# Performance work log

Measured on AMD Instinct MI355X. Metric: run time of the kernel, lower is better.

## Reference

```python
import jax, jax.numpy as jnp
import numpy as np

N_NODES = 50000
N_EDGES = 600000
N_PATHS = 3
IN_DIM = 128
OUT_DIM = 128  # out_size(16) * heads(8)
SEM_HID = 128


def setup_inputs() -> dict:
    key = jax.random.key(0)
    ks = jax.random.split(key, 8)
    h = jax.random.normal(ks[0], (N_NODES, IN_DIM), jnp.float32)
    edge_src = jax.random.randint(ks[1], (N_PATHS, N_EDGES), 0, N_NODES, dtype=jnp.int32)
    edge_dst = jax.random.randint(ks[2], (N_PATHS, N_EDGES), 0, N_NODES, dtype=jnp.int32)
    W_gc = jax.random.normal(ks[3], (N_PATHS, IN_DIM, OUT_DIM), jnp.float32) * (1.0 / np.sqrt(IN_DIM))
    b_gc = jnp.zeros((N_PATHS, OUT_DIM), jnp.float32)
    w1 = jax.random.normal(ks[4], (OUT_DIM, SEM_HID), jnp.float32) * (1.0 / np.sqrt(OUT_DIM))
    b1 = jnp.zeros((SEM_HID,), jnp.float32)
    w2 = jax.random.normal(ks[5], (SEM_HID, 1), jnp.float32) * (1.0 / np.sqrt(SEM_HID))
    return {"h": h, "W_gc": W_gc, "b_gc": b_gc, "w1": w1, "b1": b1, "w2": w2,
            "edge_src": edge_src, "edge_dst": edge_dst}


def reference(h, W_gc, b_gc, w1, b1, w2, edge_src, edge_dst):
    n = h.shape[0]

    def graph_conv(W, b, src, dst):
        # DGL GraphConv, norm='both': D_out^{-1/2} message -> sum -> D_in^{-1/2}, + bias
        ones = jnp.ones(src.shape, h.dtype)
        deg_out = jax.ops.segment_sum(ones, src, num_segments=n)
        deg_in = jax.ops.segment_sum(ones, dst, num_segments=n)
        x = h * jax.lax.rsqrt(jnp.maximum(deg_out, 1.0))[:, None]
        x = x @ W  # [N, OUT_DIM]
        agg = jax.ops.segment_sum(x[src], dst, num_segments=n)
        return agg * jax.lax.rsqrt(jnp.maximum(deg_in, 1.0))[:, None] + b

    # z: [N, P, D] stacked per-metapath embeddings
    z = jax.vmap(graph_conv, in_axes=(0, 0, 0, 0), out_axes=1)(W_gc, b_gc, edge_src, edge_dst)
    # semantic attention: mean over nodes of per-(node,path) scores
    w = jnp.mean(jnp.tanh(z @ w1 + b1) @ w2, axis=0)  # [P, 1]
    beta = jax.nn.softmax(w, axis=0)                   # [P, 1]
    return jnp.sum(beta * z, axis=1)                   # [N, D]
```

## Files before the change

kernel.cpp:

```cpp
#include <hip/hip_runtime.h>
#include <math.h>

#define N_NODES 50000
#define N_EDGES 600000
#define N_PATHS 3
#define DIM 128
#define NROWS_ALL (N_PATHS * N_NODES)
#define NE_ALL (N_PATHS * N_EDGES)
#define SCAN_BLOCKS ((NROWS_ALL + 1023) / 1024)
#define NTILES_ALL (NROWS_ALL / 16)
#define NTILES_N (N_NODES / 16)

#define HB_BINS 16384
#define HB_RANGES 4
#define HB_CHUNKS 24
#define CHUNK_E (N_EDGES / HB_CHUNKS)

typedef __attribute__((ext_vector_type(8))) short bf16x8;
typedef __attribute__((ext_vector_type(4))) float f32x4;

__device__ __forceinline__ unsigned short f2bf(float f) {
    unsigned u = __float_as_uint(f);
    u += 0x7FFF + ((u >> 16) & 1);
    return (unsigned short)(u >> 16);
}
__device__ __forceinline__ float tanh_fast(float x) {
    return 1.0f - 2.0f / (__expf(2.0f * x) + 1.0f);
}

__global__ void conv_h(const float* __restrict__ h, unsigned int* __restrict__ hb) {
    int i = blockIdx.x * blockDim.x + threadIdx.x;
    if (i >= N_NODES * DIM / 8) return;
    const float4* h4 = (const float4*)h;
    float4 a = h4[2 * i], b = h4[2 * i + 1];
    uint4 o;
    o.x = f2bf(a.x) | ((unsigned)f2bf(a.y) << 16);
    o.y = f2bf(a.z) | ((unsigned)f2bf(a.w) << 16);
    o.z = f2bf(b.x) | ((unsigned)f2bf(b.y) << 16);
    o.w = f2bf(b.z) | ((unsigned)f2bf(b.w) << 16);
    ((uint4*)hb)[i] = o;
}

__global__ void conv_w(const float* __restrict__ W_gc, const float* __restrict__ w1,
                       uint4* __restrict__ wsw) {
    int i = blockIdx.x * blockDim.x + threadIdx.x;
    if (i >= (N_PATHS + 1) * 2048) return;
    int mat = i >> 11;
    int rem = i & 2047;
    int frag = rem >> 6, lane = rem & 63;
    int n0 = frag >> 2, q = frag & 3;
    int quad = lane >> 4, m = lane & 15;
    int n = n0 * 16 + m;
    int kbase = q * 32 + quad * 8;
    const float* src = (mat < N_PATHS) ? (W_gc + (size_t)mat * DIM * DIM) : w1;
    unsigned short t[8];
#pragma unroll
    for (int j = 0; j < 8; ++j) t[j] = f2bf(src[(size_t)(kbase + j) * DIM + n]);
    uint4 o;
    o.x = t[0] | ((unsigned)t[1] << 16);
    o.y = t[2] | ((unsigned)t[3] << 16);
    o.z = t[4] | ((unsigned)t[5] << 16);
    o.w = t[6] | ((unsigned)t[7] << 16);
    wsw[i] = o;
}

__global__ __launch_bounds__(256) void hist_kernel(const int* __restrict__ esrc,
                                                   const int* __restrict__ edst,
                                                   int* __restrict__ pcnt_out,
                                                   int* __restrict__ pcnt_in) {
    __shared__ int bins[HB_BINS];
    int tid = threadIdx.x;
    {   int4* b4 = (int4*)bins;
        for (int i = tid; i < HB_BINS / 4; i += 256) b4[i] = make_int4(0, 0, 0, 0);
    }
    int b = blockIdx.x;
    int c = b % HB_CHUNKS;
    int r = (b / HB_CHUNKS) % HB_RANGES;
    int p = (b / (HB_CHUNKS * HB_RANGES)) % N_PATHS;
    int type = b / (HB_CHUNKS * HB_RANGES * N_PATHS);
    const int* ptr = (type == 0 ? esrc : edst) + (size_t)p * N_EDGES + c * CHUNK_E;
    int r0 = r * HB_BINS;
    __syncthreads();
    const int4* p4 = (const int4*)ptr;
    for (int i = tid * 2; i < CHUNK_E / 4; i += 512) {
        int4 a = p4[i];
        int4 bb = p4[i + 1];
        int l0 = a.x - r0;  if ((unsigned)l0 < HB_BINS) atomicAdd(&bins[l0], 1);
        int l1 = a.y - r0;  if ((unsigned)l1 < HB_BINS) atomicAdd(&bins[l1], 1);
        int l2 = a.z - r0;  if ((unsigned)l2 < HB_BINS) atomicAdd(&bins[l2], 1);
        int l3 = a.w - r0;  if ((unsigned)l3 < HB_BINS) atomicAdd(&bins[l3], 1);
        int l4 = bb.x - r0; if ((unsigned)l4 < HB_BINS) atomicAdd(&bins[l4], 1);
        int l5 = bb.y - r0; if ((unsigned)l5 < HB_BINS) atomicAdd(&bins[l5], 1);
        int l6 = bb.z - r0; if ((unsigned)l6 < HB_BINS) atomicAdd(&bins[l6], 1);
        int l7 = bb.w - r0; if ((unsigned)l7 < HB_BINS) atomicAdd(&bins[l7], 1);
    }
    __syncthreads();
    int bound = min(HB_BINS, N_NODES - r0);
    int* dst = (type == 0 ? pcnt_out : pcnt_in) + (size_t)c * NROWS_ALL + p * N_NODES + r0;
    const int4* b4 = (const int4*)bins;
    int4* d4 = (int4*)dst;
    for (int i = tid; i < bound / 4; i += 256) d4[i] = b4[i];
}

__global__ __launch_bounds__(256) void scan_pass1(const int* __restrict__ pcnt_out,
                                                  const int* __restrict__ pcnt_in,
                                                  int* __restrict__ cnt_out,
                                                  int* __restrict__ cnt_in,
                                                  float* __restrict__ sc_out,
                                                  int* __restrict__ partial) {
    __shared__ int lds[256];
    int t = threadIdx.x;
    int base = blockIdx.x * 1024 + t * 4;
    int4 ci = make_int4(0, 0, 0, 0);
    if (base < NROWS_ALL) {
        int4 co = make_int4(0, 0, 0, 0);
#pragma unroll
        for (int c = 0; c < HB_CHUNKS; ++c) {
            int4 vi = *(const int4*)(pcnt_in + (size_t)c * NROWS_ALL + base);
            int4 vo = *(const int4*)(pcnt_out + (size_t)c * NROWS_ALL + base);
            ci.x += vi.x; ci.y += vi.y; ci.z += vi.z; ci.w += vi.w;
            co.x += vo.x; co.y += vo.y; co.z += vo.z; co.w += vo.w;
        }
        *(int4*)(cnt_in + base) = ci;
        *(int4*)(cnt_out + base) = co;
        float4 sc;
        sc.x = rsqrtf(fmaxf((float)co.x, 1.0f));
        sc.y = rsqrtf(fmaxf((float)co.y, 1.0f));
        sc.z = rsqrtf(fmaxf((float)co.z, 1.0f));
        sc.w = rsqrtf(fmaxf((float)co.w, 1.0f));
        *(float4*)(sc_out + base) = sc;
    }
    int s = ci.x + ci.y + ci.z + ci.w;
    lds[t] = s; __syncthreads();
    for (int off = 1; off < 256; off <<= 1) {
        int u = (t >= off) ? lds[t - off] : 0;
        __syncthreads();
        lds[t] += u;
        __syncthreads();
    }
    if (t == 255) partial[blockIdx.x] = lds[255];
}

__global__ __launch_bounds__(256) void scan_pass2(int* __restrict__ partial) {
    __shared__ int lds[256];
    int t = threadIdx.x;
    int s = (t < SCAN_BLOCKS) ? partial[t] : 0;
    lds[t] = s; __syncthreads();
    for (int off = 1; off < 256; off <<= 1) {
        int u = (t >= off) ? lds[t - off] : 0;
        __syncthreads();
        lds[t] += u;
        __syncthreads();
    }
    if (t < SCAN_BLOCKS) partial[t] = lds[t] - s;
}

__global__ __launch_bounds__(256) void scan_pass3(const int* __restrict__ cnt,
                                                  const int* __restrict__ partial,
                                                  int* __restrict__ cursor,
                                                  int* __restrict__ pcnt_in) {
    __shared__ int lds[256];
    int t = threadIdx.x;
    int base = blockIdx.x * 1024 + t * 4;
    int4 v = make_int4(0, 0, 0, 0);
    if (base < NROWS_ALL) v = *(const int4*)(cnt + base);
    int s = v.x + v.y + v.z + v.w;
    lds[t] = s; __syncthreads();
    for (int off = 1; off < 256; off <<= 1) {
        int u = (t >= off) ? lds[t - off] : 0;
        __syncthreads();
        lds[t] += u;
        __syncthreads();
    }
    if (base < NROWS_ALL) {
        int run = partial[blockIdx.x] + lds[t] - s;
        int vv[4] = {v.x, v.y, v.z, v.w};
        int rb[4];
#pragma unroll
        for (int j = 0; j < 4; ++j) { cursor[base + j] = run; rb[j] = run; run += vv[j]; }
#pragma unroll
        for (int c = 0; c < HB_CHUNKS; ++c) {
            int4 pc = *(const int4*)(pcnt_in + (size_t)c * NROWS_ALL + base);
            *(int4*)(pcnt_in + (size_t)c * NROWS_ALL + base) = make_int4(rb[0], rb[1], rb[2], rb[3]);
            rb[0] += pc.x; rb[1] += pc.y; rb[2] += pc.z; rb[3] += pc.w;
        }
    }
}

__global__ __launch_bounds__(256) void fill2_kernel(const int* __restrict__ esrc,
                                                    const int* __restrict__ edst,
                                                    const int* __restrict__ pcnt_in,
                                                    unsigned short* __restrict__ col) {
    __shared__ int curs[HB_BINS];
    int tid = threadIdx.x;
    int b = blockIdx.x;
    int c = b % HB_CHUNKS;
    int r = (b / HB_CHUNKS) % HB_RANGES;
    int p = b / (HB_CHUNKS * HB_RANGES);
    int r0 = r * HB_BINS;
    int bound = min(HB_BINS, N_NODES - r0);
    const int* basep = pcnt_in + (size_t)c * NROWS_ALL + p * N_NODES + r0;
    for (int i = tid; i < bound; i += 256) curs[i] = basep[i];
    __syncthreads();
    const int4* sp4 = (const int4*)(esrc + (size_t)p * N_EDGES + c * CHUNK_E);
    const int4* dp4 = (const int4*)(edst + (size_t)p * N_EDGES + c * CHUNK_E);
    for (int i = tid * 2; i < CHUNK_E / 4; i += 512) {
        int4 dv0 = dp4[i];
        int4 dv1 = dp4[i + 1];
        int4 sv0 = sp4[i];
        int4 sv1 = sp4[i + 1];
        int l0 = dv0.x - r0; if ((unsigned)l0 < HB_BINS) { int pos = atomicAdd(&curs[l0], 1); col[pos] = (unsigned short)sv0.x; }
        int l1 = dv0.y - r0; if ((unsigned)l1 < HB_BINS) { int pos = atomicAdd(&curs[l1], 1); col[pos] = (unsigned short)sv0.y; }
        int l2 = dv0.z - r0; if ((unsigned)l2 < HB_BINS) { int pos = atomicAdd(&curs[l2], 1); col[pos] = (unsigned short)sv0.z; }
        int l3 = dv0.w - r0; if ((unsigned)l3 < HB_BINS) { int pos = atomicAdd(&curs[l3], 1); col[pos] = (unsigned short)sv0.w; }
        int l4 = dv1.x - r0; if ((unsigned)l4 < HB_BINS) { int pos = atomicAdd(&curs[l4], 1); col[pos] = (unsigned short)sv1.x; }
        int l5 = dv1.y - r0; if ((unsigned)l5 < HB_BINS) { int pos = atomicAdd(&curs[l5], 1); col[pos] = (unsigned short)sv1.y; }
        int l6 = dv1.z - r0; if ((unsigned)l6 < HB_BINS) { int pos = atomicAdd(&curs[l6], 1); col[pos] = (unsigned short)sv1.z; }
        int l7 = dv1.w - r0; if ((unsigned)l7 < HB_BINS) { int pos = atomicAdd(&curs[l7], 1); col[pos] = (unsigned short)sv1.w; }
    }
}

__global__ __launch_bounds__(256) void gather_kernel(const int* __restrict__ cursor,
                                                     const int* __restrict__ cnt_in,
                                                     const unsigned short* __restrict__ col,
                                                     const float* __restrict__ sc_out,
                                                     const uint4* __restrict__ hb4,
                                                     uint4* __restrict__ aggb4) {
    int wid = blockIdx.x * 4 + (threadIdx.x >> 6);
    int lane = threadIdx.x & 63;
    int ss = lane >> 4;
    int ln = lane & 15;
    if (wid >= NROWS_ALL) return;
    int p = wid / N_NODES;
    int beg = cursor[wid];
    int end = beg + cnt_in[wid];
    const float* scp = sc_out + p * N_NODES;
    float acc[8] = {};
    int e = beg + ss;
    for (; e + 4 < end; e += 8) {
        int s0 = col[e];
        int s1 = col[e + 4];
        float c0 = scp[s0];
        float c1 = scp[s1];
        uint4 v0 = hb4[s0 * 16 + ln];
        uint4 v1 = hb4[s1 * 16 + ln];
        acc[0] = fmaf(__uint_as_float(v0.x << 16),        c0, acc[0]);
        acc[1] = fmaf(__uint_as_float(v0.x & 0xFFFF0000u), c0, acc[1]);
        acc[2] = fmaf(__uint_as_float(v0.y << 16),        c0, acc[2]);
        acc[3] = fmaf(__uint_as_float(v0.y & 0xFFFF0000u), c0, acc[3]);
        acc[4] = fmaf(__uint_as_float(v0.z << 16),        c0, acc[4]);
        acc[5] = fmaf(__uint_as_float(v0.z & 0xFFFF0000u), c0, acc[5]);
        acc[6] = fmaf(__uint_as_float(v0.w << 16),        c0, acc[6]);
        acc[7] = fmaf(__uint_as_float(v0.w & 0xFFFF0000u), c0, acc[7]);
        acc[0] = fmaf(__uint_as_float(v1.x << 16),        c1, acc[0]);
        acc[1] = fmaf(__uint_as_float(v1.x & 0xFFFF0000u), c1, acc[1]);
        acc[2] = fmaf(__uint_as_float(v1.y << 16),        c1, acc[2]);
        acc[3] = fmaf(__uint_as_float(v1.y & 0xFFFF0000u), c1, acc[3]);
        acc[4] = fmaf(__uint_as_float(v1.z << 16),        c1, acc[4]);
        acc[5] = fmaf(__uint_as_float(v1.z & 0xFFFF0000u), c1, acc[5]);
        acc[6] = fmaf(__uint_as_float(v1.w << 16),        c1, acc[6]);
        acc[7] = fmaf(__uint_as_float(v1.w & 0xFFFF0000u), c1, acc[7]);
    }
    if (e < end) {
        int s0 = col[e];
        float c0 = scp[s0];
        uint4 v0 = hb4[s0 * 16 + ln];
        acc[0] = fmaf(__uint_as_float(v0.x << 16),        c0, acc[0]);
        acc[1] = fmaf(__uint_as_float(v0.x & 0xFFFF0000u), c0, acc[1]);
        acc[2] = fmaf(__uint_as_float(v0.y << 16),        c0, acc[2]);
        acc[3] = fmaf(__uint_as_float(v0.y & 0xFFFF0000u), c0, acc[3]);
        acc[4] = fmaf(__uint_as_float(v0.z << 16),        c0, acc[4]);
        acc[5] = fmaf(__uint_as_float(v0.z & 0xFFFF0000u), c0, acc[5]);
        acc[6] = fmaf(__uint_as_float(v0.w << 16),        c0, acc[6]);
        acc[7] = fmaf(__uint_as_float(v0.w & 0xFFFF0000u), c0, acc[7]);
    }
#pragma unroll
    for (int j = 0; j < 8; ++j) {
        acc[j] += __shfl_xor(acc[j], 16, 64);
        acc[j] += __shfl_xor(acc[j], 32, 64);
    }
    if (ss == 0) {
        uint4 o;
        o.x = f2bf(acc[0]) | ((unsigned)f2bf(acc[1]) << 16);
        o.y = f2bf(acc[2]) | ((unsigned)f2bf(acc[3]) << 16);
        o.z = f2bf(acc[4]) | ((unsigned)f2bf(acc[5]) << 16);
        o.w = f2bf(acc[6]) | ((unsigned)f2bf(acc[7]) << 16);
        int t = wid >> 4, m = wid & 15, q = ln >> 2, qd = ln & 3;
        aggb4[(size_t)t * 256 + q * 64 + qd * 16 + m] = o;
    }
}

__global__ __launch_bounds__(256, 4) void score_pass(const uint4* __restrict__ aggb4,
                                                     const uint4* __restrict__ wsw,
                                                     const int* __restrict__ cnt_in,
                                                     const float* __restrict__ b_gc,
                                                     const float* __restrict__ b1,
                                                     const float* __restrict__ w2,
                                                     float* __restrict__ scorep) {
    __shared__ float zS[4][16][132];
    int wave = threadIdx.x >> 6, lane = threadIdx.x & 63;
    int m = lane & 15, quad = lane >> 4;
    int t = blockIdx.x * 4 + wave;
    if (t >= NTILES_ALL) return;
    int r0 = t * 16;
    int p = r0 / N_NODES;
    const uint4* At = aggb4 + (size_t)t * 256 + lane;
    bf16x8 a[4];
#pragma unroll
    for (int q = 0; q < 4; ++q) a[q] = *(const bf16x8*)&At[q * 64];
    float s[4];
#pragma unroll
    for (int rg = 0; rg < 4; ++rg)
        s[rg] = rsqrtf(fmaxf((float)cnt_in[r0 + quad * 4 + rg], 1.0f));
    const uint4* Bp = wsw + (size_t)p * 2048 + lane;
    const float* bgc = b_gc + p * DIM;
    float (*zw)[132] = zS[wave];
#pragma unroll
    for (int n0 = 0; n0 < 8; ++n0) {
        f32x4 acc = {0.f, 0.f, 0.f, 0.f};
#pragma unroll
        for (int q = 0; q < 4; ++q) {
            bf16x8 b = *(const bf16x8*)&Bp[(n0 * 4 + q) * 64];
            acc = __builtin_amdgcn_mfma_f32_16x16x32_bf16(a[q], b, acc, 0, 0, 0);
        }
        int colj = n0 * 16 + m;
        float bias = bgc[colj];
#pragma unroll
        for (int rg = 0; rg < 4; ++rg)
            zw[quad * 4 + rg][colj] = acc[rg] * s[rg] + bias;
    }
    bf16x8 sa[4];
#pragma unroll
    for (int q = 0; q < 4; ++q) {
        const float* pr = &zw[m][q * 32 + quad * 8];
        float4 f0 = *(const float4*)pr;
        float4 f1 = *(const float4*)(pr + 4);
        bf16x8 tt;
        tt[0] = f2bf(f0.x); tt[1] = f2bf(f0.y); tt[2] = f2bf(f0.z); tt[3] = f2bf(f0.w);
        tt[4] = f2bf(f1.x); tt[5] = f2bf(f1.y); tt[6] = f2bf(f1.z); tt[7] = f2bf(f1.w);
        sa[q] = tt;
    }
    const uint4* W1 = wsw + (size_t)N_PATHS * 2048 + lane;
    float rsum[4] = {0.f, 0.f, 0.f, 0.f};
#pragma unroll
    for (int n0 = 0; n0 < 8; ++n0) {
        f32x4 acc = {0.f, 0.f, 0.f, 0.f};
#pragma unroll
        for (int q = 0; q < 4; ++q) {
            bf16x8 b = *(const bf16x8*)&W1[(n0 * 4 + q) * 64];
            acc = __builtin_amdgcn_mfma_f32_16x16x32_bf16(sa[q], b, acc, 0, 0, 0);
        }
        int colj = n0 * 16 + m;
        float bj = b1[colj], wj = w2[colj];
#pragma unroll
        for (int rg = 0; rg < 4; ++rg)
            rsum[rg] += tanh_fast(acc[rg] + bj) * wj;
    }
#pragma unroll
    for (int off = 1; off < 64; off <<= 1)
#pragma unroll
        for (int rg = 0; rg < 4; ++rg) rsum[rg] += __shfl_xor(rsum[rg], off, 64);
    if (lane == 0)
        scorep[t] = rsum[0] + rsum[1] + rsum[2] + rsum[3];
}

__global__ __launch_bounds__(1024) void beta_kernel(const float* __restrict__ scorep,
                                                    float* __restrict__ beta) {
    __shared__ float red[3][1024];
    int t = threadIdx.x;
    float a0 = 0.f, a1 = 0.f, a2 = 0.f;
    for (int i = t; i < NTILES_ALL; i += 1024) {
        float v = scorep[i];
        int p = (i * 16) / N_NODES;
        if (p == 0) a0 += v; else if (p == 1) a1 += v; else a2 += v;
    }
    red[0][t] = a0; red[1][t] = a1; red[2][t] = a2;
    __syncthreads();
    for (int off = 512; off > 0; off >>= 1) {
        if (t < off) {
            red[0][t] += red[0][t + off];
            red[1][t] += red[1][t + off];
            red[2][t] += red[2][t + off];
        }
        __syncthreads();
    }
    if (t == 0) {
        float a = red[0][0] / (float)N_NODES;
        float b = red[1][0] / (float)N_NODES;
        float c = red[2][0] / (float)N_NODES;
        float mx = fmaxf(a, fmaxf(b, c));
        float e0 = expf(a - mx), e1 = expf(b - mx), e2 = expf(c - mx);
        float sm = e0 + e1 + e2;
        beta[0] = e0 / sm; beta[1] = e1 / sm; beta[2] = e2 / sm;
    }
}

__global__ __launch_bounds__(256, 4) void out_pass(const uint4* __restrict__ aggb4,
                                                   const uint4* __restrict__ wsw,
                                                   const int* __restrict__ cnt_in,
                                                   const float* __restrict__ b_gc,
                                                   const float* __restrict__ beta,
                                                   float* __restrict__ out) {
    __shared__ float zS[4][16][132];
    int wave = threadIdx.x >> 6, lane = threadIdx.x & 63;
    int m = lane & 15, quad = lane >> 4;
    int t = blockIdx.x * 4 + wave;
    if (t >= NTILES_N) return;
    int r0 = t * 16;
    float of[8][4] = {};
#pragma unroll
    for (int p = 0; p < N_PATHS; ++p) {
        const uint4* At = aggb4 + (size_t)(p * NTILES_N + t) * 256 + lane;
        bf16x8 a[4];
#pragma unroll
        for (int q = 0; q < 4; ++q) a[q] = *(const bf16x8*)&At[q * 64];
        float s[4];
#pragma unroll
        for (int rg = 0; rg < 4; ++rg)
            s[rg] = rsqrtf(fmaxf((float)cnt_in[p * N_NODES + r0 + quad * 4 + rg], 1.0f));
        float bp = beta[p];
        const uint4* Bp = wsw + (size_t)p * 2048 + lane;
        const float* bgc = b_gc + p * DIM;
#pragma unroll
        for (int n0 = 0; n0 < 8; ++n0) {
            f32x4 acc = {0.f, 0.f, 0.f, 0.f};
#pragma unroll
            for (int q = 0; q < 4; ++q) {
                bf16x8 b = *(const bf16x8*)&Bp[(n0 * 4 + q) * 64];
                acc = __builtin_amdgcn_mfma_f32_16x16x32_bf16(a[q], b, acc, 0, 0, 0);
            }
            float bias = bgc[n0 * 16 + m];
#pragma unroll
            for (int rg = 0; rg < 4; ++rg)
                of[n0][rg] = fmaf(bp, acc[rg] * s[rg] + bias, of[n0][rg]);
        }
    }
    float (*zw)[132] = zS[wave];
#pragma unroll
    for (int n0 = 0; n0 < 8; ++n0)
#pragma unroll
        for (int rg = 0; rg < 4; ++rg)
            zw[quad * 4 + rg][n0 * 16 + m] = of[n0][rg];
#pragma unroll
    for (int i = 0; i < 8; ++i) {
        int fi = i * 64 + lane;
        int row = fi >> 5, c4 = fi & 31;
        float4 v = *(const float4*)&zw[row][c4 * 4];
        *(float4*)(out + (size_t)(r0 + row) * DIM + c4 * 4) = v;
    }
}

extern "C" void kernel_launch(void* const* d_in, const int* in_sizes, int n_in,
                              void* d_out, int out_size, void* d_ws, size_t ws_size,
                              hipStream_t stream) {
    const float* h    = (const float*)d_in[0];
    const float* W_gc = (const float*)d_in[1];
    const float* b_gc = (const float*)d_in[2];
    const float* w1   = (const float*)d_in[3];
    const float* b1   = (const float*)d_in[4];
    const float* w2   = (const float*)d_in[5];
    const int* esrc   = (const int*)d_in[6];
    const int* edst   = (const int*)d_in[7];
    float* out        = (float*)d_out;

    int*   cnt_out = (int*)d_ws;
    int*   cnt_in  = cnt_out + NROWS_ALL;
    float* beta    = (float*)d_ws + 300004;
    int*   partial = (int*)d_ws + 300032;
    float* sc_out  = (float*)d_ws + 300288;
    float* scorep  = (float*)d_ws + 300288;
    uint4* wsw     = (uint4*)((int*)d_ws + 450288);
    unsigned int* aggb = (unsigned int*)((int*)d_ws + 483056);
    int*   cursor  = (int*)d_ws + 10083056;
    unsigned short* col = (unsigned short*)((int*)d_ws + 10233056);
    unsigned int*   hb  = (unsigned int*)((int*)d_ws + 11133056);
    int*   pcnt_out = (int*)d_ws + 14333056;
    int*   pcnt_in  = (int*)d_ws + 17933056;

    conv_h<<<(N_NODES * DIM / 8 + 255) / 256, 256, 0, stream>>>(h, hb);
    conv_w<<<((N_PATHS + 1) * 2048 + 255) / 256, 256, 0, stream>>>(W_gc, w1, wsw);

    hist_kernel<<<2 * N_PATHS * HB_RANGES * HB_CHUNKS, 256, 0, stream>>>(
        esrc, edst, pcnt_out, pcnt_in);

    scan_pass1<<<SCAN_BLOCKS, 256, 0, stream>>>(
        pcnt_out, pcnt_in, cnt_out, cnt_in, sc_out, partial);
    scan_pass2<<<1, 256, 0, stream>>>(partial);
    scan_pass3<<<SCAN_BLOCKS, 256, 0, stream>>>(cnt_in, partial, cursor, pcnt_in);

    fill2_kernel<<<N_PATHS * HB_RANGES * HB_CHUNKS, 256, 0, stream>>>(
        esrc, edst, pcnt_in, col);

    gather_kernel<<<(NROWS_ALL + 3) / 4, 256, 0, stream>>>(
        cursor, cnt_in, col, sc_out, (const uint4*)hb, (uint4*)aggb);

    score_pass<<<(NTILES_ALL + 3) / 4, 256, 0, stream>>>(
        (const uint4*)aggb, wsw, cnt_in, b_gc, b1, w2, scorep);

    beta_kernel<<<1, 1024, 0, stream>>>(scorep, beta);

    out_pass<<<(NTILES_N + 3) / 4, 256, 0, stream>>>(
        (const uint4*)aggb, wsw, cnt_in, b_gc, beta, out);
}
```

Before: 280.7 us.

## Pack src index with fp16 norm scale into CSR, pack histogram bins, split gather rows

The histogram kernel now packs two 16-bit counters per 32-bit shared word, which halves the number of range passes over the edge lists. The fill kernel stores each source index together with its fp16 out-degree scale in one 32-bit CSR entry, so the gather no longer does a separate dependent lookup into sc_out. The gather splits each destination row across two waves that each handle half the feature columns, with eight edge lanes per wave. In exchange, the scale drops to fp16 precision and fill does extra random reads into sc_out.

```diff
diff --git a/kernel.cpp b/kernel.cpp
--- a/kernel.cpp
+++ b/kernel.cpp
@@ -1,4 +1,5 @@
 #include <hip/hip_runtime.h>
+#include <hip/hip_fp16.h>
 #include <math.h>
 
 #define N_NODES 50000
@@ -11,10 +12,12 @@
 #define NTILES_ALL (NROWS_ALL / 16)
 #define NTILES_N (N_NODES / 16)
 
-#define HB_BINS 16384
-#define HB_RANGES 4
 #define HB_CHUNKS 24
 #define CHUNK_E (N_EDGES / HB_CHUNKS)
+#define H2_BINS 32768
+#define H2_RANGES 2
+#define HF_BINS 16384
+#define HF_RANGES 4
 
 typedef __attribute__((ext_vector_type(8))) short bf16x8;
 typedef __attribute__((ext_vector_type(4))) float f32x4;
@@ -68,38 +71,41 @@
                                                    const int* __restrict__ edst,
                                                    int* __restrict__ pcnt_out,
                                                    int* __restrict__ pcnt_in) {
-    __shared__ int bins[HB_BINS];
+    __shared__ unsigned bins32[H2_BINS / 2];
     int tid = threadIdx.x;
-    {   int4* b4 = (int4*)bins;
-        for (int i = tid; i < HB_BINS / 4; i += 256) b4[i] = make_int4(0, 0, 0, 0);
+    {   uint4* b4 = (uint4*)bins32;
+        for (int i = tid; i < H2_BINS / 8; i += 256) b4[i] = make_uint4(0, 0, 0, 0);
     }
     int b = blockIdx.x;
     int c = b % HB_CHUNKS;
-    int r = (b / HB_CHUNKS) % HB_RANGES;
-    int p = (b / (HB_CHUNKS * HB_RANGES)) % N_PATHS;
-    int type = b / (HB_CHUNKS * HB_RANGES * N_PATHS);
+    int r = (b / HB_CHUNKS) % H2_RANGES;
+    int p = (b / (HB_CHUNKS * H2_RANGES)) % N_PATHS;
+    int type = b / (HB_CHUNKS * H2_RANGES * N_PATHS);
     const int* ptr = (type == 0 ? esrc : edst) + (size_t)p * N_EDGES + c * CHUNK_E;
-    int r0 = r * HB_BINS;
+    int r0 = r * H2_BINS;
     __syncthreads();
     const int4* p4 = (const int4*)ptr;
     for (int i = tid * 2; i < CHUNK_E / 4; i += 512) {
         int4 a = p4[i];
         int4 bb = p4[i + 1];
-        int l0 = a.x - r0;  if ((unsigned)l0 < HB_BINS) atomicAdd(&bins[l0], 1);
-        int l1 = a.y - r0;  if ((unsigned)l1 < HB_BINS) atomicAdd(&bins[l1], 1);
-        int l2 = a.z - r0;  if ((unsigned)l2 < HB_BINS) atomicAdd(&bins[l2], 1);
-        int l3 = a.w - r0;  if ((unsigned)l3 < HB_BINS) atomicAdd(&bins[l3], 1);
-        int l4 = bb.x - r0; if ((unsigned)l4 < HB_BINS) atomicAdd(&bins[l4], 1);
-        int l5 = bb.y - r0; if ((unsigned)l5 < HB_BINS) atomicAdd(&bins[l5], 1);
-        int l6 = bb.z - r0; if ((unsigned)l6 < HB_BINS) atomicAdd(&bins[l6], 1);
-        int l7 = bb.w - r0; if ((unsigned)l7 < HB_BINS) atomicAdd(&bins[l7], 1);
+        int l;
+        l = a.x - r0;  if ((unsigned)l < H2_BINS) atomicAdd(&bins32[l >> 1], 1u << ((l & 1) << 4));
+        l = a.y - r0;  if ((unsigned)l < H2_BINS) atomicAdd(&bins32[l >> 1], 1u << ((l & 1) << 4));
+        l = a.z - r0;  if ((unsigned)l < H2_BINS) atomicAdd(&bins32[l >> 1], 1u << ((l & 1) << 4));
+        l = a.w - r0;  if ((unsigned)l < H2_BINS) atomicAdd(&bins32[l >> 1], 1u << ((l & 1) << 4));
+        l = bb.x - r0; if ((unsigned)l < H2_BINS) atomicAdd(&bins32[l >> 1], 1u << ((l & 1) << 4));
+        l = bb.y - r0; if ((unsigned)l < H2_BINS) atomicAdd(&bins32[l >> 1], 1u << ((l & 1) << 4));
+        l = bb.z - r0; if ((unsigned)l < H2_BINS) atomicAdd(&bins32[l >> 1], 1u << ((l & 1) << 4));
+        l = bb.w - r0; if ((unsigned)l < H2_BINS) atomicAdd(&bins32[l >> 1], 1u << ((l & 1) << 4));
     }
     __syncthreads();
-    int bound = min(HB_BINS, N_NODES - r0);
+    int bound = min(H2_BINS, N_NODES - r0);
     int* dst = (type == 0 ? pcnt_out : pcnt_in) + (size_t)c * NROWS_ALL + p * N_NODES + r0;
-    const int4* b4 = (const int4*)bins;
-    int4* d4 = (int4*)dst;
-    for (int i = tid; i < bound / 4; i += 256) d4[i] = b4[i];
+    for (int j = tid; j < bound / 2; j += 256) {
+        unsigned u = bins32[j];
+        int2 w = make_int2((int)(u & 0xFFFFu), (int)(u >> 16));
+        *(int2*)(dst + 2 * j) = w;
+    }
 }
 
 __global__ __launch_bounds__(256) void scan_pass1(const int* __restrict__ pcnt_out,
@@ -190,18 +196,20 @@
 __global__ __launch_bounds__(256) void fill2_kernel(const int* __restrict__ esrc,
                                                     const int* __restrict__ edst,
                                                     const int* __restrict__ pcnt_in,
-                                                    unsigned short* __restrict__ col) {
-    __shared__ int curs[HB_BINS];
+                                                    const float* __restrict__ sc_out,
+                                                    unsigned int* __restrict__ colsc) {
+    __shared__ int curs[HF_BINS];
     int tid = threadIdx.x;
     int b = blockIdx.x;
     int c = b % HB_CHUNKS;
-    int r = (b / HB_CHUNKS) % HB_RANGES;
-    int p = b / (HB_CHUNKS * HB_RANGES);
-    int r0 = r * HB_BINS;
-    int bound = min(HB_BINS, N_NODES - r0);
+    int r = (b / HB_CHUNKS) % HF_RANGES;
+    int p = b / (HB_CHUNKS * HF_RANGES);
+    int r0 = r * HF_BINS;
+    int bound = min(HF_BINS, N_NODES - r0);
     const int* basep = pcnt_in + (size_t)c * NROWS_ALL + p * N_NODES + r0;
     for (int i = tid; i < bound; i += 256) curs[i] = basep[i];
     __syncthreads();
+    const float* scp = sc_out + p * N_NODES;
     const int4* sp4 = (const int4*)(esrc + (size_t)p * N_EDGES + c * CHUNK_E);
     const int4* dp4 = (const int4*)(edst + (size_t)p * N_EDGES + c * CHUNK_E);
     for (int i = tid * 2; i < CHUNK_E / 4; i += 512) {
@@ -209,73 +217,50 @@
         int4 dv1 = dp4[i + 1];
         int4 sv0 = sp4[i];
         int4 sv1 = sp4[i + 1];
-        int l0 = dv0.x - r0; if ((unsigned)l0 < HB_BINS) { int pos = atomicAdd(&curs[l0], 1); col[pos] = (unsigned short)sv0.x; }
-        int l1 = dv0.y - r0; if ((unsigned)l1 < HB_BINS) { int pos = atomicAdd(&curs[l1], 1); col[pos] = (unsigned short)sv0.y; }
-        int l2 = dv0.z - r0; if ((unsigned)l2 < HB_BINS) { int pos = atomicAdd(&curs[l2], 1); col[pos] = (unsigned short)sv0.z; }
-        int l3 = dv0.w - r0; if ((unsigned)l3 < HB_BINS) { int pos = atomicAdd(&curs[l3], 1); col[pos] = (unsigned short)sv0.w; }
-        int l4 = dv1.x - r0; if ((unsigned)l4 < HB_BINS) { int pos = atomicAdd(&curs[l4], 1); col[pos] = (unsigned short)sv1.x; }
-        int l5 = dv1.y - r0; if ((unsigned)l5 < HB_BINS) { int pos = atomicAdd(&curs[l5], 1); col[pos] = (unsigned short)sv1.y; }
-        int l6 = dv1.z - r0; if ((unsigned)l6 < HB_BINS) { int pos = atomicAdd(&curs[l6], 1); col[pos] = (unsigned short)sv1.z; }
-        int l7 = dv1.w - r0; if ((unsigned)l7 < HB_BINS) { int pos = atomicAdd(&curs[l7], 1); col[pos] = (unsigned short)sv1.w; }
+        int l;
+        l = dv0.x - r0; if ((unsigned)l < HF_BINS) { int pos = atomicAdd(&curs[l], 1); colsc[pos] = (unsigned)sv0.x | ((unsigned)__half_as_ushort(__float2half(scp[sv0.x])) << 16); }
+        l = dv0.y - r0; if ((unsigned)l < HF_BINS) { int pos = atomicAdd(&curs[l], 1); colsc[pos] = (unsigned)sv0.y | ((unsigned)__half_as_ushort(__float2half(scp[sv0.y])) << 16); }
+        l = dv0.z - r0; if ((unsigned)l < HF_BINS) { int pos = atomicAdd(&curs[l], 1); colsc[pos] = (unsigned)sv0.z | ((unsigned)__half_as_ushort(__float2half(scp[sv0.z])) << 16); }
+        l = dv0.w - r0; if ((unsigned)l < HF_BINS) { int pos = atomicAdd(&curs[l], 1); colsc[pos] = (unsigned)sv0.w | ((unsigned)__half_as_ushort(__float2half(scp[sv0.w])) << 16); }
+        l = dv1.x - r0; if ((unsigned)l < HF_BINS) { int pos = atomicAdd(&curs[l], 1); colsc[pos] = (unsigned)sv1.x | ((unsigned)__half_as_ushort(__float2half(scp[sv1.x])) << 16); }
+        l = dv1.y - r0; if ((unsigned)l < HF_BINS) { int pos = atomicAdd(&curs[l], 1); colsc[pos] = (unsigned)sv1.y | ((unsigned)__half_as_ushort(__float2half(scp[sv1.y])) << 16); }
+        l = dv1.z - r0; if ((unsigned)l < HF_BINS) { int pos = atomicAdd(&curs[l], 1); colsc[pos] = (unsigned)sv1.z | ((unsigned)__half_as_ushort(__float2half(scp[sv1.z])) << 16); }
+        l = dv1.w - r0; if ((unsigned)l < HF_BINS) { int pos = atomicAdd(&curs[l], 1); colsc[pos] = (unsigned)sv1.w | ((unsigned)__half_as_ushort(__float2half(scp[sv1.w])) << 16); }
     }
 }
 
 __global__ __launch_bounds__(256) void gather_kernel(const int* __restrict__ cursor,
                                                      const int* __restrict__ cnt_in,
-                                                     const unsigned short* __restrict__ col,
-                                                     const float* __restrict__ sc_out,
+                                                     const unsigned int* __restrict__ colsc,
                                                      const uint4* __restrict__ hb4,
                                                      uint4* __restrict__ aggb4) {
-    int wid = blockIdx.x * 4 + (threadIdx.x >> 6);
-    int lane = threadIdx.x & 63;
-    int ss = lane >> 4;
-    int ln = lane & 15;
+    int wave = threadIdx.x >> 6, lane = threadIdx.x & 63;
+    int wid = blockIdx.x * 2 + (wave >> 1);
+    int dh = wave & 1;
+    int ss = lane >> 3;
+    int ln = lane & 7;
     if (wid >= NROWS_ALL) return;
-    int p = wid / N_NODES;
     int beg = cursor[wid];
     int end = beg + cnt_in[wid];
-    const float* scp = sc_out + p * N_NODES;
+    int idx = dh * 8 + ln;
     float acc[8] = {};
-    int e = beg + ss;
-    for (; e + 4 < end; e += 8) {
-        int s0 = col[e];
-        int s1 = col[e + 4];
-        float c0 = scp[s0];
-        float c1 = scp[s1];
-        uint4 v0 = hb4[s0 * 16 + ln];
-        uint4 v1 = hb4[s1 * 16 + ln];
-        acc[0] = fmaf(__uint_as_float(v0.x << 16),        c0, acc[0]);
-        acc[1] = fmaf(__uint_as_float(v0.x & 0xFFFF0000u), c0, acc[1]);
-        acc[2] = fmaf(__uint_as_float(v0.y << 16),        c0, acc[2]);
-        acc[3] = fmaf(__uint_as_float(v0.y & 0xFFFF0000u), c0, acc[3]);
-        acc[4] = fmaf(__uint_as_float(v0.z << 16),        c0, acc[4]);
-        acc[5] = fmaf(__uint_as_float(v0.z & 0xFFFF0000u), c0, acc[5]);
-        acc[6] = fmaf(__uint_as_float(v0.w << 16),        c0, acc[6]);
-        acc[7] = fmaf(__uint_as_float(v0.w & 0xFFFF0000u), c0, acc[7]);
-        acc[0] = fmaf(__uint_as_float(v1.x << 16),        c1, acc[0]);
-        acc[1] = fmaf(__uint_as_float(v1.x & 0xFFFF0000u), c1, acc[1]);
-        acc[2] = fmaf(__uint_as_float(v1.y << 16),        c1, acc[2]);
-        acc[3] = fmaf(__uint_as_float(v1.y & 0xFFFF0000u), c1, acc[3]);
-        acc[4] = fmaf(__uint_as_float(v1.z << 16),        c1, acc[4]);
-        acc[5] = fmaf(__uint_as_float(v1.z & 0xFFFF0000u), c1, acc[5]);
-        acc[6] = fmaf(__uint_as_float(v1.w << 16),        c1, acc[6]);
-        acc[7] = fmaf(__uint_as_float(v1.w & 0xFFFF0000u), c1, acc[7]);
-    }
-    if (e < end) {
-        int s0 = col[e];
-        float c0 = scp[s0];
-        uint4 v0 = hb4[s0 * 16 + ln];
-        acc[0] = fmaf(__uint_as_float(v0.x << 16),        c0, acc[0]);
-        acc[1] = fmaf(__uint_as_float(v0.x & 0xFFFF0000u), c0, acc[1]);
-        acc[2] = fmaf(__uint_as_float(v0.y << 16),        c0, acc[2]);
-        acc[3] = fmaf(__uint_as_float(v0.y & 0xFFFF0000u), c0, acc[3]);
-        acc[4] = fmaf(__uint_as_float(v0.z << 16),        c0, acc[4]);
-        acc[5] = fmaf(__uint_as_float(v0.z & 0xFFFF0000u), c0, acc[5]);
-        acc[6] = fmaf(__uint_as_float(v0.w << 16),        c0, acc[6]);
-        acc[7] = fmaf(__uint_as_float(v0.w & 0xFFFF0000u), c0, acc[7]);
+    for (int e = beg + ss; e < end; e += 8) {
+        unsigned cs = colsc[e];
+        int s = cs & 0xFFFF;
+        float sc = __half2float(__ushort_as_half((unsigned short)(cs >> 16)));
+        uint4 v = hb4[s * 16 + idx];
+        acc[0] = fmaf(__uint_as_float(v.x << 16),        sc, acc[0]);
+        acc[1] = fmaf(__uint_as_float(v.x & 0xFFFF0000u), sc, acc[1]);
+        acc[2] = fmaf(__uint_as_float(v.y << 16),        sc, acc[2]);
+        acc[3] = fmaf(__uint_as_float(v.y & 0xFFFF0000u), sc, acc[3]);
+        acc[4] = fmaf(__uint_as_float(v.z << 16),        sc, acc[4]);
+        acc[5] = fmaf(__uint_as_float(v.z & 0xFFFF0000u), sc, acc[5]);
+        acc[6] = fmaf(__uint_as_float(v.w << 16),        sc, acc[6]);
+        acc[7] = fmaf(__uint_as_float(v.w & 0xFFFF0000u), sc, acc[7]);
     }
 #pragma unroll
     for (int j = 0; j < 8; ++j) {
+        acc[j] += __shfl_xor(acc[j], 8, 64);
         acc[j] += __shfl_xor(acc[j], 16, 64);
         acc[j] += __shfl_xor(acc[j], 32, 64);
     }
@@ -285,8 +270,8 @@
         o.y = f2bf(acc[2]) | ((unsigned)f2bf(acc[3]) << 16);
         o.z = f2bf(acc[4]) | ((unsigned)f2bf(acc[5]) << 16);
         o.w = f2bf(acc[6]) | ((unsigned)f2bf(acc[7]) << 16);
-        int t = wid >> 4, m = wid & 15, q = ln >> 2, qd = ln & 3;
-        aggb4[(size_t)t * 256 + q * 64 + qd * 16 + m] = o;
+        int t = wid >> 4, m = wid & 15;
+        aggb4[(size_t)t * 256 + idx * 16 + m] = o;
     }
 }
 
@@ -471,16 +456,16 @@
     float* scorep  = (float*)d_ws + 300288;
     uint4* wsw     = (uint4*)((int*)d_ws + 450288);
     unsigned int* aggb = (unsigned int*)((int*)d_ws + 483056);
-    int*   cursor  = (int*)d_ws + 10083056;
-    unsigned short* col = (unsigned short*)((int*)d_ws + 10233056);
-    unsigned int*   hb  = (unsigned int*)((int*)d_ws + 11133056);
-    int*   pcnt_out = (int*)d_ws + 14333056;
-    int*   pcnt_in  = (int*)d_ws + 17933056;
+    int*   cursor  = (int*)d_ws + 10233056;
+    unsigned int* colsc = (unsigned int*)((int*)d_ws + 10383056);
+    unsigned int* hb    = (unsigned int*)((int*)d_ws + 12183056);
+    int*   pcnt_out = (int*)d_ws + 15383056;
+    int*   pcnt_in  = (int*)d_ws + 18983056;
 
     conv_h<<<(N_NODES * DIM / 8 + 255) / 256, 256, 0, stream>>>(h, hb);
     conv_w<<<((N_PATHS + 1) * 2048 + 255) / 256, 256, 0, stream>>>(W_gc, w1, wsw);
 
-    hist_kernel<<<2 * N_PATHS * HB_RANGES * HB_CHUNKS, 256, 0, stream>>>(
+    hist_kernel<<<2 * N_PATHS * H2_RANGES * HB_CHUNKS, 256, 0, stream>>>(
         esrc, edst, pcnt_out, pcnt_in);
 
     scan_pass1<<<SCAN_BLOCKS, 256, 0, stream>>>(
@@ -488,11 +473,11 @@
     scan_pass2<<<1, 256, 0, stream>>>(partial);
     scan_pass3<<<SCAN_BLOCKS, 256, 0, stream>>>(cnt_in, partial, cursor, pcnt_in);
 
-    fill2_kernel<<<N_PATHS * HB_RANGES * HB_CHUNKS, 256, 0, stream>>>(
-        esrc, edst, pcnt_in, col);
-
-    gather_kernel<<<(NROWS_ALL + 3) / 4, 256, 0, stream>>>(
-        cursor, cnt_in, col, sc_out, (const uint4*)hb, (uint4*)aggb);
+    fill2_kernel<<<N_PATHS * HF_RANGES * HB_CHUNKS, 256, 0, stream>>>(
+        esrc, edst, pcnt_in, sc_out, colsc);
+
+    gather_kernel<<<(NROWS_ALL + 1) / 2, 256, 0, stream>>>(
+        cursor, cnt_in, colsc, (const uint4*)hb, (uint4*)aggb);
 
     score_pass<<<(NTILES_ALL + 3) / 4, 256, 0, stream>>>(
         (const uint4*)aggb, wsw, cnt_in, b_gc, b1, w2, scorep);
```

Result: slower. 347.2 us (+23.7%).
